# Kernel tuning notes

Measured on AMD Instinct MI355X. Metric: run time of the kernel, lower is better.

The kernel has to match this reference:

```python
import jax, jax.numpy as jnp
import numpy as np

HEADS = 4
DIM_HEAD = 32
CHUNK = 1024
GROUPS = 8
EPS = 1e-5


def setup_inputs() -> dict:
    key = jax.random.key(0)
    k1, k2, k3 = jax.random.split(key, 3)
    b, dim, h, w = 8, 64, 96, 96
    inner = HEADS * DIM_HEAD  # 128
    x = jax.random.normal(k1, (b, dim, h, w), dtype=jnp.float32)
    W_qkv = jax.random.normal(k2, (3 * inner, dim), dtype=jnp.float32) * (1.0 / np.sqrt(dim))
    W_out = jax.random.normal(k3, (dim, inner), dtype=jnp.float32) * (1.0 / np.sqrt(inner))
    b_out = jnp.zeros((dim,), dtype=jnp.float32)
    gamma = jnp.ones((dim,), dtype=jnp.float32)
    beta = jnp.zeros((dim,), dtype=jnp.float32)
    return {"x": x, "W_qkv": W_qkv, "W_out": W_out, "b_out": b_out,
            "gamma": gamma, "beta": beta}


def reference(x, W_qkv, W_out, b_out, gamma, beta):
    b, c, h, w = x.shape
    n = h * w
    nch = n // CHUNK  # number of full chunks (n chosen divisible by CHUNK)
    d = DIM_HEAD
    BH = b * HEADS

    # 1x1 conv (no bias) == matmul over channel dim
    xf = x.reshape(b, c, n)
    qkv = jnp.einsum('oc,bcn->bon', W_qkv, xf)          # [b, 3*inner, n]
    q, k, v = jnp.split(qkv, 3, axis=1)                  # each [b, inner, n]

    def chunkify(t):
        # [b, inner, n] -> [BH, nch, d, CHUNK]; slicing i:i+CHUNK on last axis
        # equals reshaping n -> (nch, CHUNK) in order.
        return t.reshape(BH, d, nch, CHUNK).transpose(0, 2, 1, 3)

    qc, kc, vc = chunkify(q), chunkify(k), chunkify(v)

    qs = jax.nn.softmax(qc, axis=-1)  # softmax over chunk spatial positions
    ks = jax.nn.softmax(kc, axis=-2)  # softmax over head channels

    # context = k_chunk^T @ v_chunk : [BH, nch, CHUNK, CHUNK]
    ctx = jnp.einsum('gkdi,gkdj->gkij', ks, vc)
    # chunk_out = q_chunk @ context : [BH, nch, d, CHUNK]
    out = jnp.einsum('gkdi,gkij->gkdj', qs, ctx)

    # concat chunks back along spatial dim, reshape to image layout
    out = out.transpose(0, 2, 1, 3).reshape(b, HEADS * d, h, w)

    # to_out: 1x1 conv with bias, then GroupNorm(8, dim)
    y = jnp.einsum('oc,bchw->bohw', W_out, out) + b_out[None, :, None, None]

    yg = y.reshape(b, GROUPS, c // GROUPS, h, w)
    mu = jnp.mean(yg, axis=(2, 3, 4), keepdims=True)
    var = jnp.var(yg, axis=(2, 3, 4), keepdims=True)
    yn = ((yg - mu) * jax.lax.rsqrt(var + EPS)).reshape(b, c, h, w)
    return yn * gamma[None, :, None, None] + beta[None, :, None, None]
```

## Files before the change

kernel.cpp:

```cpp
#include <hip/hip_runtime.h>
#include <hip/hip_bf16.h>

#define N_POS 9216
#define NCHUNK 9
#define BATCH 8
#define CDIM 64
#define HEADS 4
#define EPS 1e-5f

#define PPART_SZ ((size_t)32 * NCHUNK * 1024)
#define NPART 8
#define MP_SLICE ((size_t)(BATCH * NCHUNK) * 4096)
#define WBF_BYTES ((size_t)384 * 64 * 2)

typedef __attribute__((ext_vector_type(8))) short short8;
typedef __attribute__((ext_vector_type(4))) float f32x4;

static __device__ inline unsigned pk2(float a, float b) {
    __hip_bfloat162 h2(__float2bfloat16(a), __float2bfloat16(b));
    return *reinterpret_cast<unsigned*>(&h2);
}
static __device__ inline float bf2f(short s) {
    union { unsigned u; float f; } c; c.u = ((unsigned)(unsigned short)s) << 16; return c.f;
}

__global__ __launch_bounds__(256) void wprep_kernel(const float* __restrict__ Wqkv,
        __hip_bfloat16* __restrict__ wbf, float* __restrict__ stats) {
    int i = blockIdx.x * 256 + threadIdx.x;
    if (i < 6144) {
        float4 v = ((const float4*)Wqkv)[i];
        uint2 u; u.x = pk2(v.x, v.y); u.y = pk2(v.z, v.w);
        ((uint2*)wbf)[i] = u;
    }
    if (i < 128) stats[i] = 0.f;
}

__global__ __launch_bounds__(256) void qkp_kernel(const float* __restrict__ x,
        const __hip_bfloat16* __restrict__ wbf, float* __restrict__ Pparts) {
    int bx = blockIdx.x;
    int b  = blockIdx.y;
    int ck = bx >> 3, pt = bx & 7;
    __shared__ __align__(16) char lraw[36864];
    __hip_bfloat16 (*xs)[72]  = (__hip_bfloat16(*)[72])lraw;
    __hip_bfloat16 (*skT)[72] = (__hip_bfloat16(*)[72])lraw;
    int t = threadIdx.x, w = t >> 6, l = t & 63;
    int l15 = l & 15, quad = l >> 4;

    f32x4 pac[2][2];
    pac[0][0] = (f32x4){0,0,0,0}; pac[0][1] = (f32x4){0,0,0,0};
    pac[1][0] = (f32x4){0,0,0,0}; pac[1][1] = (f32x4){0,0,0,0};

    for (int half = 0; half < 2; ++half) {
        int n0 = bx * 128 + half * 64;
        {
            int p = t & 63, cbase = (t >> 6) * 16;
            const float* xb = x + (size_t)b * CDIM * N_POS + n0 + p;
            #pragma unroll
            for (int j = 0; j < 16; j += 4) {
                float v0 = xb[(size_t)(cbase + j + 0) * N_POS];
                float v1 = xb[(size_t)(cbase + j + 1) * N_POS];
                float v2 = xb[(size_t)(cbase + j + 2) * N_POS];
                float v3 = xb[(size_t)(cbase + j + 3) * N_POS];
                uint2 u; u.x = pk2(v0, v1); u.y = pk2(v2, v3);
                *reinterpret_cast<uint2*>(&xs[p][cbase + j]) = u;
            }
        }
        __syncthreads();

        f32x4 acc[4][4];
        #pragma unroll
        for (int mt = 0; mt < 4; ++mt)
            #pragma unroll
            for (int nt = 0; nt < 4; ++nt) acc[mt][nt] = (f32x4){0.f, 0.f, 0.f, 0.f};
        #pragma unroll
        for (int ks = 0; ks < 2; ++ks) {
            int k0 = ks * 32 + quad * 8;
            short8 av[4];
            #pragma unroll
            for (int mt = 0; mt < 4; ++mt)
                av[mt] = *reinterpret_cast<const short8*>(&xs[mt * 16 + l15][k0]);
            #pragma unroll
            for (int nt = 0; nt < 4; ++nt) {
                short8 bw = *reinterpret_cast<const short8*>(wbf + (size_t)(w * 64 + nt * 16 + l15) * 64 + k0);
                #pragma unroll
                for (int mt = 0; mt < 4; ++mt)
                    acc[mt][nt] = __builtin_amdgcn_mfma_f32_16x16x32_bf16(av[mt], bw, acc[mt][nt], 0, 0, 0);
            }
        }
        __syncthreads();

        if (w < 2) {
            #pragma unroll
            for (int nt = 0; nt < 4; ++nt) {
                int ch = w * 64 + nt * 16 + l15;
                #pragma unroll
                for (int mt = 0; mt < 4; ++mt) {
                    uint2 u;
                    u.x = pk2(__expf(acc[mt][nt][0]), __expf(acc[mt][nt][1]));
                    u.y = pk2(__expf(acc[mt][nt][2]), __expf(acc[mt][nt][3]));
                    *reinterpret_cast<uint2*>(&skT[ch][mt * 16 + quad * 4]) = u;
                }
            }
        } else {
            #pragma unroll
            for (int nt = 0; nt < 4; ++nt) {
                int ch = w * 64 + nt * 16 + l15;
                #pragma unroll
                for (int mt = 0; mt < 4; ++mt) {
                    uint2 u;
                    u.x = pk2(acc[mt][nt][0], acc[mt][nt][1]);
                    u.y = pk2(acc[mt][nt][2], acc[mt][nt][3]);
                    *reinterpret_cast<uint2*>(&skT[ch][mt * 16 + quad * 4]) = u;
                }
            }
        }
        __syncthreads();

        {
            int p = t & 63, h = t >> 6;
            float kr[32]; float mx = -1e30f;
            #pragma unroll
            for (int d = 0; d < 32; ++d) { kr[d] = bf2f(*(const short*)&skT[128 + h * 32 + d][p]); mx = fmaxf(mx, kr[d]); }
            float s = 0.f;
            #pragma unroll
            for (int d = 0; d < 32; ++d) { kr[d] = __expf(kr[d] - mx); s += kr[d]; }
            float is = 1.f / s;
            #pragma unroll
            for (int d = 0; d < 32; ++d) skT[128 + h * 32 + d][p] = __float2bfloat16(kr[d] * is);
        }
        __syncthreads();

        #pragma unroll
        for (int step = 0; step < 2; ++step) {
            int k0 = step * 32 + quad * 8;
            short8 bk[2];
            #pragma unroll
            for (int nt = 0; nt < 2; ++nt)
                bk[nt] = *reinterpret_cast<const short8*>(&skT[128 + w * 32 + nt * 16 + l15][k0]);
            #pragma unroll
            for (int mt = 0; mt < 2; ++mt) {
                short8 aq = *reinterpret_cast<const short8*>(&skT[w * 32 + mt * 16 + l15][k0]);
                pac[mt][0] = __builtin_amdgcn_mfma_f32_16x16x32_bf16(aq, bk[0], pac[mt][0], 0, 0, 0);
                pac[mt][1] = __builtin_amdgcn_mfma_f32_16x16x32_bf16(aq, bk[1], pac[mt][1], 0, 0, 0);
            }
        }
        __syncthreads();
    }

    float* Pp = Pparts + (size_t)pt * PPART_SZ + ((size_t)(b * 4 + w) * NCHUNK + ck) * 1024;
    #pragma unroll
    for (int mt = 0; mt < 2; ++mt)
        #pragma unroll
        for (int nt = 0; nt < 2; ++nt)
            #pragma unroll
            for (int r = 0; r < 4; ++r)
                Pp[(mt * 16 + quad * 4 + r) * 32 + nt * 16 + l15] = pac[mt][nt][r];
}

__global__ __launch_bounds__(256) void umat_kernel(const float* __restrict__ Wout,
        const float* __restrict__ Wqkv, const float* __restrict__ Pparts,
        float* __restrict__ Mp) {
    int ck = blockIdx.x, b = blockIdx.y, h = blockIdx.z;
    int bh = b * 4 + h;
    int t = threadIdx.x;
    __shared__ float Pl[32][32];
    __shared__ float iZ[32];
    __shared__ float Ul[64][33];
    __shared__ float Wvh[32][68];
    size_t base4 = ((size_t)bh * NCHUNK + ck) * 256;
    {
        const float4* P0 = (const float4*)Pparts + base4 + t;
        float4 s = (float4){0.f, 0.f, 0.f, 0.f};
        #pragma unroll
        for (int j = 0; j < NPART; ++j) {
            float4 a = P0[j * (PPART_SZ / 4)];
            s.x += a.x; s.y += a.y; s.z += a.z; s.w += a.w;
        }
        ((float4*)Pl)[t] = s;
    }
    {
        int e = t >> 3, cq = t & 7;
        const float4* wr = (const float4*)(Wqkv + (size_t)(256 + h * 32 + e) * 64 + cq * 8);
        float4 a0 = wr[0], a1 = wr[1];
        *reinterpret_cast<float4*>(&Wvh[e][cq * 8])     = a0;
        *reinterpret_cast<float4*>(&Wvh[e][cq * 8 + 4]) = a1;
    }
    __syncthreads();
    if (t < 32) {
        float s = 0.f;
        #pragma unroll
        for (int c = 0; c < 32; ++c) s += Pl[t][c];
        iZ[t] = 1.f / s;
    }
    __syncthreads();
    int o = t & 63, wv = t >> 6;
    float wz[32];
    {
        const float4* wr = (const float4*)(Wout + (size_t)o * 128 + h * 32);
        #pragma unroll
        for (int j = 0; j < 8; ++j) {
            float4 f = wr[j];
            wz[j*4+0] = f.x * iZ[j*4+0]; wz[j*4+1] = f.y * iZ[j*4+1];
            wz[j*4+2] = f.z * iZ[j*4+2]; wz[j*4+3] = f.w * iZ[j*4+3];
        }
    }
    float ua[8];
    #pragma unroll
    for (int j = 0; j < 8; ++j) ua[j] = 0.f;
    for (int d = 0; d < 32; ++d) {
        float wd = wz[d];
        #pragma unroll
        for (int j = 0; j < 8; ++j) ua[j] += wd * Pl[d][wv * 8 + j];
    }
    #pragma unroll
    for (int j = 0; j < 8; ++j) Ul[o][wv * 8 + j] = ua[j];
    __syncthreads();

    float macc[16];
    #pragma unroll
    for (int j = 0; j < 16; ++j) macc[j] = 0.f;
    for (int e = 0; e < 32; ++e) {
        float u = Ul[o][e];
        const float4* wvp = reinterpret_cast<const float4*>(&Wvh[e][wv * 16]);
        #pragma unroll
        for (int q = 0; q < 4; ++q) {
            float4 f = wvp[q];
            macc[q*4+0] += u * f.x; macc[q*4+1] += u * f.y;
            macc[q*4+2] += u * f.z; macc[q*4+3] += u * f.w;
        }
    }
    float* mp = Mp + (size_t)h * MP_SLICE + ((size_t)(b * NCHUNK + ck)) * 4096
              + (size_t)o * 64 + wv * 16;
    #pragma unroll
    for (int q = 0; q < 4; ++q) {
        float4 f; f.x = macc[q*4+0]; f.y = macc[q*4+1]; f.z = macc[q*4+2]; f.w = macc[q*4+3];
        reinterpret_cast<float4*>(mp)[q] = f;
    }
}

__global__ __launch_bounds__(256) void y_kernel(const float* __restrict__ x,
        const float* __restrict__ Mp, const float* __restrict__ bout,
        __hip_bfloat16* __restrict__ ybf, float* __restrict__ stats) {
    int bx = blockIdx.x;
    int b  = blockIdx.y;
    int ck = bx >> 3;
    int n0 = bx * 128;
    __shared__ __align__(16) __hip_bfloat16 xs[128][72];
    __shared__ __align__(16) __hip_bfloat16 Ml[64][72];
    __shared__ float gsum[8], gsq[8];
    int t = threadIdx.x, w = t >> 6, l = t & 63;
    int l15 = l & 15, quad = l >> 4;
    if (t < 8) { gsum[t] = 0.f; gsq[t] = 0.f; }

    {
        int p = t & 127, cbase = (t >> 7) * 32;
        const float* xb = x + (size_t)b * CDIM * N_POS + n0 + p;
        #pragma unroll
        for (int j = 0; j < 32; j += 4) {
            float v0 = xb[(size_t)(cbase + j + 0) * N_POS];
            float v1 = xb[(size_t)(cbase + j + 1) * N_POS];
            float v2 = xb[(size_t)(cbase + j + 2) * N_POS];
            float v3 = xb[(size_t)(cbase + j + 3) * N_POS];
            uint2 u; u.x = pk2(v0, v1); u.y = pk2(v2, v3);
            *reinterpret_cast<uint2*>(&xs[p][cbase + j]) = u;
        }
    }
    {
        int o = t >> 2, cs = (t & 3) * 16;
        const float* mb = Mp + ((size_t)(b * NCHUNK + ck)) * 4096 + (size_t)o * 64 + cs;
        float m[16];
        #pragma unroll
        for (int q = 0; q < 4; ++q) {
            float4 f = reinterpret_cast<const float4*>(mb)[q];
            m[q*4+0] = f.x; m[q*4+1] = f.y; m[q*4+2] = f.z; m[q*4+3] = f.w;
        }
        #pragma unroll
        for (int h = 1; h < 4; ++h) {
            const float* mh = mb + h * MP_SLICE;
            #pragma unroll
            for (int q = 0; q < 4; ++q) {
                float4 f = reinterpret_cast<const float4*>(mh)[q];
                m[q*4+0] += f.x; m[q*4+1] += f.y; m[q*4+2] += f.z; m[q*4+3] += f.w;
            }
        }
        #pragma unroll
        for (int q = 0; q < 4; ++q) {
            uint2 u; u.x = pk2(m[q*4+0], m[q*4+1]); u.y = pk2(m[q*4+2], m[q*4+3]);
            *reinterpret_cast<uint2*>(&Ml[o][cs + q * 4]) = u;
        }
    }
    __syncthreads();

    int nw = w * 32;
    f32x4 acc[4][2];
    #pragma unroll
    for (int mt = 0; mt < 4; ++mt) { acc[mt][0] = (f32x4){0,0,0,0}; acc[mt][1] = (f32x4){0,0,0,0}; }
    #pragma unroll
    for (int ks = 0; ks < 2; ++ks) {
        int k0 = ks * 32 + quad * 8;
        short8 bf[2];
        #pragma unroll
        for (int nt = 0; nt < 2; ++nt)
            bf[nt] = *reinterpret_cast<const short8*>(&xs[nw + nt * 16 + l15][k0]);
        #pragma unroll
        for (int mt = 0; mt < 4; ++mt) {
            short8 af = *reinterpret_cast<const short8*>(&Ml[mt * 16 + l15][k0]);
            acc[mt][0] = __builtin_amdgcn_mfma_f32_16x16x32_bf16(af, bf[0], acc[mt][0], 0, 0, 0);
            acc[mt][1] = __builtin_amdgcn_mfma_f32_16x16x32_bf16(af, bf[1], acc[mt][1], 0, 0, 0);
        }
    }
    float gsl[4], gql[4];
    #pragma unroll
    for (int mt = 0; mt < 4; ++mt) { gsl[mt] = 0.f; gql[mt] = 0.f; }
    __hip_bfloat16* yb = ybf + (size_t)b * CDIM * N_POS;
    int nbase = n0 + nw;
    #pragma unroll
    for (int mt = 0; mt < 4; ++mt) {
        float4 bo = *reinterpret_cast<const float4*>(bout + mt * 16 + quad * 4);
        const float* bop = reinterpret_cast<const float*>(&bo);
        #pragma unroll
        for (int nt = 0; nt < 2; ++nt) {
            int n = nbase + nt * 16 + l15;
            #pragma unroll
            for (int r = 0; r < 4; ++r) {
                int o = mt * 16 + quad * 4 + r;
                float val = acc[mt][nt][r] + bop[r];
                yb[(size_t)o * N_POS + n] = __float2bfloat16(val);
                gsl[mt] += val; gql[mt] += val * val;
            }
        }
    }
    #pragma unroll
    for (int off = 16; off >= 1; off >>= 1) {
        #pragma unroll
        for (int mt = 0; mt < 4; ++mt) {
            gsl[mt] += __shfl_xor(gsl[mt], off, 64);
            gql[mt] += __shfl_xor(gql[mt], off, 64);
        }
    }
    if (l == 0 || l == 32) {
        int qh = quad >> 1;
        #pragma unroll
        for (int mt = 0; mt < 4; ++mt) {
            atomicAdd(&gsum[2 * mt + qh], gsl[mt]);
            atomicAdd(&gsq[2 * mt + qh], gql[mt]);
        }
    }
    __syncthreads();
    if (t < 8) {
        atomicAdd(&stats[(b * 8 + t) * 2],     gsum[t]);
        atomicAdd(&stats[(b * 8 + t) * 2 + 1], gsq[t]);
    }
}

__global__ __launch_bounds__(256) void gn_kernel(const __hip_bfloat16* __restrict__ ybf,
        float* __restrict__ out, const float* __restrict__ stats,
        const float* __restrict__ gamma, const float* __restrict__ beta) {
    int bc = blockIdx.y;
    int c = bc & 63, b = bc >> 6;
    int g = c >> 3;
    float s = stats[(b * 8 + g) * 2], q = stats[(b * 8 + g) * 2 + 1];
    const float invN = 1.f / (8.f * N_POS);
    float mean = s * invN;
    float var = q * invN - mean * mean;
    float sc = rsqrtf(var + EPS);
    float ga = gamma[c] * sc;
    float be = beta[c] - mean * sc * gamma[c];
    size_t base = ((size_t)b * CDIM + c) * N_POS + (size_t)(blockIdx.x * 256 + threadIdx.x) * 4;
    uint2 u = *reinterpret_cast<const uint2*>(ybf + base);
    float4 v;
    v.x = bf2f((short)(u.x & 0xffff)); v.y = bf2f((short)(u.x >> 16));
    v.z = bf2f((short)(u.y & 0xffff)); v.w = bf2f((short)(u.y >> 16));
    v.x = v.x * ga + be; v.y = v.y * ga + be; v.z = v.z * ga + be; v.w = v.w * ga + be;
    *reinterpret_cast<float4*>(out + base) = v;
}

extern "C" void kernel_launch(void* const* d_in, const int* in_sizes, int n_in,
                              void* d_out, int out_size, void* d_ws, size_t ws_size,
                              hipStream_t stream) {
    const float* x     = (const float*)d_in[0];
    const float* Wqkv  = (const float*)d_in[1];
    const float* Wout  = (const float*)d_in[2];
    const float* bout  = (const float*)d_in[3];
    const float* gamma = (const float*)d_in[4];
    const float* beta  = (const float*)d_in[5];
    float* out = (float*)d_out;

    float* stats  = (float*)d_ws;
    float* Pparts = stats + 128;
    float* Mp     = Pparts + NPART * PPART_SZ;
    __hip_bfloat16* wbf = (__hip_bfloat16*)(Mp + 4 * MP_SLICE);
    __hip_bfloat16* ybf = (__hip_bfloat16*)((char*)wbf + WBF_BYTES);

    wprep_kernel<<<dim3(24), 256, 0, stream>>>(Wqkv, wbf, stats);
    qkp_kernel<<<dim3(72, BATCH), 256, 0, stream>>>(x, wbf, Pparts);
    umat_kernel<<<dim3(NCHUNK, BATCH, HEADS), 256, 0, stream>>>(Wout, Wqkv, Pparts, Mp);
    y_kernel<<<dim3(72, BATCH), 256, 0, stream>>>(x, Mp, bout, ybf, stats);
    gn_kernel<<<dim3(9, 512), 256, 0, stream>>>(ybf, out, stats, gamma, beta);
}
```

Before: 125.4 us.

## Load MFMA operands directly from global into registers and double qkp grid

qkp_kernel now gives each block 64 positions instead of 128, so its grid doubles and the partial-sum count goes from 8 to 16. Each wave loads its x fragment straight into MFMA registers, skipping the LDS staging pass. The k channel softmax is now done in registers with cross-lane shuffles rather than a separate LDS pass, and the partial buffer layout is reorganised to match. y_kernel likewise builds its M and x fragments directly from global memory without LDS, trading shared-memory traffic and barriers for uncoalesced strided global loads and redundant loads of M across waves.

Result: slower. 154.5 us (+23.3%).

```diff
diff --git a/kernel.cpp b/kernel.cpp
--- a/kernel.cpp
+++ b/kernel.cpp
@@ -8,8 +8,8 @@
 #define HEADS 4
 #define EPS 1e-5f
 
-#define PPART_SZ ((size_t)32 * NCHUNK * 1024)
-#define NPART 8
+#define NPART 16
+#define PPARTS_TOT ((size_t)BATCH * NCHUNK * NPART * 4096)
 #define MP_SLICE ((size_t)(BATCH * NCHUNK) * 4096)
 #define WBF_BYTES ((size_t)384 * 64 * 2)
 
@@ -22,6 +22,10 @@
 }
 static __device__ inline float bf2f(short s) {
     union { unsigned u; float f; } c; c.u = ((unsigned)(unsigned short)s) << 16; return c.f;
+}
+static __device__ inline short8 mk8(unsigned a, unsigned b, unsigned c, unsigned d) {
+    union { short8 s; unsigned u[4]; } cv;
+    cv.u[0] = a; cv.u[1] = b; cv.u[2] = c; cv.u[3] = d; return cv.s;
 }
 
 __global__ __launch_bounds__(256) void wprep_kernel(const float* __restrict__ Wqkv,
@@ -39,141 +43,115 @@
         const __hip_bfloat16* __restrict__ wbf, float* __restrict__ Pparts) {
     int bx = blockIdx.x;
     int b  = blockIdx.y;
-    int ck = bx >> 3, pt = bx & 7;
-    __shared__ __align__(16) char lraw[36864];
-    __hip_bfloat16 (*xs)[72]  = (__hip_bfloat16(*)[72])lraw;
-    __hip_bfloat16 (*skT)[72] = (__hip_bfloat16(*)[72])lraw;
+    int ck = bx >> 4, pt = bx & 15;
+    __shared__ __align__(16) __hip_bfloat16 skT[256][72];
     int t = threadIdx.x, w = t >> 6, l = t & 63;
     int l15 = l & 15, quad = l >> 4;
+    int p0 = bx * 64 + w * 16;
+
+    short8 afr[2];
+    {
+        const float* xb = x + (size_t)b * CDIM * N_POS + p0 + l15;
+        #pragma unroll
+        for (int ks = 0; ks < 2; ++ks) {
+            float v[8];
+            #pragma unroll
+            for (int j = 0; j < 8; ++j)
+                v[j] = xb[(size_t)(ks * 32 + quad * 8 + j) * N_POS];
+            afr[ks] = mk8(pk2(v[0], v[1]), pk2(v[2], v[3]),
+                          pk2(v[4], v[5]), pk2(v[6], v[7]));
+        }
+    }
+
+    f32x4 acc[16];
+    #pragma unroll
+    for (int nt = 0; nt < 16; ++nt) acc[nt] = (f32x4){0.f, 0.f, 0.f, 0.f};
+    #pragma unroll
+    for (int ks = 0; ks < 2; ++ks) {
+        #pragma unroll
+        for (int nt = 0; nt < 16; ++nt) {
+            short8 bw = *reinterpret_cast<const short8*>(
+                wbf + (size_t)(nt * 16 + l15) * 64 + ks * 32 + quad * 8);
+            acc[nt] = __builtin_amdgcn_mfma_f32_16x16x32_bf16(afr[ks], bw, acc[nt], 0, 0, 0);
+        }
+    }
+
+    #pragma unroll
+    for (int nt = 0; nt < 8; ++nt) {
+        uint2 u;
+        u.x = pk2(__expf(acc[nt][0]), __expf(acc[nt][1]));
+        u.y = pk2(__expf(acc[nt][2]), __expf(acc[nt][3]));
+        *reinterpret_cast<uint2*>(&skT[nt * 16 + l15][w * 16 + quad * 4]) = u;
+    }
+    #pragma unroll
+    for (int h = 0; h < 4; ++h) {
+        f32x4 a0 = acc[8 + 2 * h], a1 = acc[9 + 2 * h];
+        f32x4 e0, e1;
+        #pragma unroll
+        for (int r = 0; r < 4; ++r) {
+            float m = fmaxf(a0[r], a1[r]);
+            m = fmaxf(m, __shfl_xor(m, 1));
+            m = fmaxf(m, __shfl_xor(m, 2));
+            m = fmaxf(m, __shfl_xor(m, 4));
+            m = fmaxf(m, __shfl_xor(m, 8));
+            float x0 = __expf(a0[r] - m), x1 = __expf(a1[r] - m);
+            float s = x0 + x1;
+            s += __shfl_xor(s, 1);
+            s += __shfl_xor(s, 2);
+            s += __shfl_xor(s, 4);
+            s += __shfl_xor(s, 8);
+            float is = 1.f / s;
+            e0[r] = x0 * is; e1[r] = x1 * is;
+        }
+        uint2 u;
+        u.x = pk2(e0[0], e0[1]); u.y = pk2(e0[2], e0[3]);
+        *reinterpret_cast<uint2*>(&skT[128 + h * 32 + l15][w * 16 + quad * 4]) = u;
+        u.x = pk2(e1[0], e1[1]); u.y = pk2(e1[2], e1[3]);
+        *reinterpret_cast<uint2*>(&skT[128 + h * 32 + 16 + l15][w * 16 + quad * 4]) = u;
+    }
+    __syncthreads();
 
     f32x4 pac[2][2];
     pac[0][0] = (f32x4){0,0,0,0}; pac[0][1] = (f32x4){0,0,0,0};
     pac[1][0] = (f32x4){0,0,0,0}; pac[1][1] = (f32x4){0,0,0,0};
-
-    for (int half = 0; half < 2; ++half) {
-        int n0 = bx * 128 + half * 64;
-        {
-            int p = t & 63, cbase = (t >> 6) * 16;
-            const float* xb = x + (size_t)b * CDIM * N_POS + n0 + p;
-            #pragma unroll
-            for (int j = 0; j < 16; j += 4) {
-                float v0 = xb[(size_t)(cbase + j + 0) * N_POS];
-                float v1 = xb[(size_t)(cbase + j + 1) * N_POS];
-                float v2 = xb[(size_t)(cbase + j + 2) * N_POS];
-                float v3 = xb[(size_t)(cbase + j + 3) * N_POS];
-                uint2 u; u.x = pk2(v0, v1); u.y = pk2(v2, v3);
-                *reinterpret_cast<uint2*>(&xs[p][cbase + j]) = u;
-            }
-        }
-        __syncthreads();
-
-        f32x4 acc[4][4];
-        #pragma unroll
-        for (int mt = 0; mt < 4; ++mt)
-            #pragma unroll
-            for (int nt = 0; nt < 4; ++nt) acc[mt][nt] = (f32x4){0.f, 0.f, 0.f, 0.f};
-        #pragma unroll
-        for (int ks = 0; ks < 2; ++ks) {
-            int k0 = ks * 32 + quad * 8;
-            short8 av[4];
-            #pragma unroll
-            for (int mt = 0; mt < 4; ++mt)
-                av[mt] = *reinterpret_cast<const short8*>(&xs[mt * 16 + l15][k0]);
-            #pragma unroll
-            for (int nt = 0; nt < 4; ++nt) {
-                short8 bw = *reinterpret_cast<const short8*>(wbf + (size_t)(w * 64 + nt * 16 + l15) * 64 + k0);
-                #pragma unroll
-                for (int mt = 0; mt < 4; ++mt)
-                    acc[mt][nt] = __builtin_amdgcn_mfma_f32_16x16x32_bf16(av[mt], bw, acc[mt][nt], 0, 0, 0);
-            }
-        }
-        __syncthreads();
-
-        if (w < 2) {
-            #pragma unroll
-            for (int nt = 0; nt < 4; ++nt) {
-                int ch = w * 64 + nt * 16 + l15;
-                #pragma unroll
-                for (int mt = 0; mt < 4; ++mt) {
-                    uint2 u;
-                    u.x = pk2(__expf(acc[mt][nt][0]), __expf(acc[mt][nt][1]));
-                    u.y = pk2(__expf(acc[mt][nt][2]), __expf(acc[mt][nt][3]));
-                    *reinterpret_cast<uint2*>(&skT[ch][mt * 16 + quad * 4]) = u;
-                }
-            }
-        } else {
-            #pragma unroll
-            for (int nt = 0; nt < 4; ++nt) {
-                int ch = w * 64 + nt * 16 + l15;
-                #pragma unroll
-                for (int mt = 0; mt < 4; ++mt) {
-                    uint2 u;
-                    u.x = pk2(acc[mt][nt][0], acc[mt][nt][1]);
-                    u.y = pk2(acc[mt][nt][2], acc[mt][nt][3]);
-                    *reinterpret_cast<uint2*>(&skT[ch][mt * 16 + quad * 4]) = u;
-                }
-            }
-        }
-        __syncthreads();
-
-        {
-            int p = t & 63, h = t >> 6;
-            float kr[32]; float mx = -1e30f;
-            #pragma unroll
-            for (int d = 0; d < 32; ++d) { kr[d] = bf2f(*(const short*)&skT[128 + h * 32 + d][p]); mx = fmaxf(mx, kr[d]); }
-            float s = 0.f;
-            #pragma unroll
-            for (int d = 0; d < 32; ++d) { kr[d] = __expf(kr[d] - mx); s += kr[d]; }
-            float is = 1.f / s;
-            #pragma unroll
-            for (int d = 0; d < 32; ++d) skT[128 + h * 32 + d][p] = __float2bfloat16(kr[d] * is);
-        }
-        __syncthreads();
-
-        #pragma unroll
-        for (int step = 0; step < 2; ++step) {
-            int k0 = step * 32 + quad * 8;
-            short8 bk[2];
-            #pragma unroll
-            for (int nt = 0; nt < 2; ++nt)
-                bk[nt] = *reinterpret_cast<const short8*>(&skT[128 + w * 32 + nt * 16 + l15][k0]);
-            #pragma unroll
-            for (int mt = 0; mt < 2; ++mt) {
-                short8 aq = *reinterpret_cast<const short8*>(&skT[w * 32 + mt * 16 + l15][k0]);
-                pac[mt][0] = __builtin_amdgcn_mfma_f32_16x16x32_bf16(aq, bk[0], pac[mt][0], 0, 0, 0);
-                pac[mt][1] = __builtin_amdgcn_mfma_f32_16x16x32_bf16(aq, bk[1], pac[mt][1], 0, 0, 0);
-            }
-        }
-        __syncthreads();
-    }
-
-    float* Pp = Pparts + (size_t)pt * PPART_SZ + ((size_t)(b * 4 + w) * NCHUNK + ck) * 1024;
-    #pragma unroll
-    for (int mt = 0; mt < 2; ++mt)
-        #pragma unroll
-        for (int nt = 0; nt < 2; ++nt)
+    #pragma unroll
+    for (int ks = 0; ks < 2; ++ks) {
+        int k0 = ks * 32 + quad * 8;
+        short8 aq0 = *reinterpret_cast<const short8*>(&skT[w * 32 + l15][k0]);
+        short8 aq1 = *reinterpret_cast<const short8*>(&skT[w * 32 + 16 + l15][k0]);
+        short8 bk0 = *reinterpret_cast<const short8*>(&skT[128 + w * 32 + l15][k0]);
+        short8 bk1 = *reinterpret_cast<const short8*>(&skT[128 + w * 32 + 16 + l15][k0]);
+        pac[0][0] = __builtin_amdgcn_mfma_f32_16x16x32_bf16(aq0, bk0, pac[0][0], 0, 0, 0);
+        pac[0][1] = __builtin_amdgcn_mfma_f32_16x16x32_bf16(aq0, bk1, pac[0][1], 0, 0, 0);
+        pac[1][0] = __builtin_amdgcn_mfma_f32_16x16x32_bf16(aq1, bk0, pac[1][0], 0, 0, 0);
+        pac[1][1] = __builtin_amdgcn_mfma_f32_16x16x32_bf16(aq1, bk1, pac[1][1], 0, 0, 0);
+    }
+    float* Pp = Pparts + (((size_t)(b * NCHUNK + ck) * NPART + pt) * 4 + w) * 1024;
+    #pragma unroll
+    for (int tA = 0; tA < 2; ++tA)
+        #pragma unroll
+        for (int tB = 0; tB < 2; ++tB)
             #pragma unroll
             for (int r = 0; r < 4; ++r)
-                Pp[(mt * 16 + quad * 4 + r) * 32 + nt * 16 + l15] = pac[mt][nt][r];
+                Pp[(tA * 16 + quad * 4 + r) * 32 + tB * 16 + l15] = pac[tA][tB][r];
 }
 
 __global__ __launch_bounds__(256) void umat_kernel(const float* __restrict__ Wout,
         const float* __restrict__ Wqkv, const float* __restrict__ Pparts,
         float* __restrict__ Mp) {
     int ck = blockIdx.x, b = blockIdx.y, h = blockIdx.z;
-    int bh = b * 4 + h;
     int t = threadIdx.x;
     __shared__ float Pl[32][32];
     __shared__ float iZ[32];
     __shared__ float Ul[64][33];
     __shared__ float Wvh[32][68];
-    size_t base4 = ((size_t)bh * NCHUNK + ck) * 256;
-    {
-        const float4* P0 = (const float4*)Pparts + base4 + t;
+    {
+        const float4* P0 = (const float4*)Pparts
+            + ((size_t)(b * NCHUNK + ck) * NPART) * 1024 + h * 256 + t;
         float4 s = (float4){0.f, 0.f, 0.f, 0.f};
         #pragma unroll
-        for (int j = 0; j < NPART; ++j) {
-            float4 a = P0[j * (PPART_SZ / 4)];
+        for (int pt = 0; pt < NPART; ++pt) {
+            float4 a = P0[pt * 1024];
             s.x += a.x; s.y += a.y; s.z += a.z; s.w += a.w;
         }
         ((float4*)Pl)[t] = s;
@@ -245,75 +223,65 @@
     int b  = blockIdx.y;
     int ck = bx >> 3;
     int n0 = bx * 128;
-    __shared__ __align__(16) __hip_bfloat16 xs[128][72];
-    __shared__ __align__(16) __hip_bfloat16 Ml[64][72];
     __shared__ float gsum[8], gsq[8];
     int t = threadIdx.x, w = t >> 6, l = t & 63;
     int l15 = l & 15, quad = l >> 4;
     if (t < 8) { gsum[t] = 0.f; gsq[t] = 0.f; }
-
-    {
-        int p = t & 127, cbase = (t >> 7) * 32;
-        const float* xb = x + (size_t)b * CDIM * N_POS + n0 + p;
-        #pragma unroll
-        for (int j = 0; j < 32; j += 4) {
-            float v0 = xb[(size_t)(cbase + j + 0) * N_POS];
-            float v1 = xb[(size_t)(cbase + j + 1) * N_POS];
-            float v2 = xb[(size_t)(cbase + j + 2) * N_POS];
-            float v3 = xb[(size_t)(cbase + j + 3) * N_POS];
-            uint2 u; u.x = pk2(v0, v1); u.y = pk2(v2, v3);
-            *reinterpret_cast<uint2*>(&xs[p][cbase + j]) = u;
-        }
-    }
-    {
-        int o = t >> 2, cs = (t & 3) * 16;
-        const float* mb = Mp + ((size_t)(b * NCHUNK + ck)) * 4096 + (size_t)o * 64 + cs;
-        float m[16];
-        #pragma unroll
-        for (int q = 0; q < 4; ++q) {
-            float4 f = reinterpret_cast<const float4*>(mb)[q];
-            m[q*4+0] = f.x; m[q*4+1] = f.y; m[q*4+2] = f.z; m[q*4+3] = f.w;
-        }
-        #pragma unroll
-        for (int h = 1; h < 4; ++h) {
-            const float* mh = mb + h * MP_SLICE;
-            #pragma unroll
-            for (int q = 0; q < 4; ++q) {
-                float4 f = reinterpret_cast<const float4*>(mh)[q];
-                m[q*4+0] += f.x; m[q*4+1] += f.y; m[q*4+2] += f.z; m[q*4+3] += f.w;
+    __syncthreads();
+
+    short8 mf[4][2];
+    {
+        const float* Mb = Mp + (size_t)(b * NCHUNK + ck) * 4096;
+        #pragma unroll
+        for (int mt = 0; mt < 4; ++mt)
+            #pragma unroll
+            for (int ks = 0; ks < 2; ++ks) {
+                const float* m0 = Mb + (size_t)(mt * 16 + l15) * 64 + ks * 32 + quad * 8;
+                float4 s0 = *reinterpret_cast<const float4*>(m0);
+                float4 s1 = *reinterpret_cast<const float4*>(m0 + 4);
+                #pragma unroll
+                for (int h = 1; h < 4; ++h) {
+                    const float* mh = m0 + (size_t)h * MP_SLICE;
+                    float4 a0 = *reinterpret_cast<const float4*>(mh);
+                    float4 a1 = *reinterpret_cast<const float4*>(mh + 4);
+                    s0.x += a0.x; s0.y += a0.y; s0.z += a0.z; s0.w += a0.w;
+                    s1.x += a1.x; s1.y += a1.y; s1.z += a1.z; s1.w += a1.w;
+                }
+                mf[mt][ks] = mk8(pk2(s0.x, s0.y), pk2(s0.z, s0.w),
+                                 pk2(s1.x, s1.y), pk2(s1.z, s1.w));
             }
-        }
-        #pragma unroll
-        for (int q = 0; q < 4; ++q) {
-            uint2 u; u.x = pk2(m[q*4+0], m[q*4+1]); u.y = pk2(m[q*4+2], m[q*4+3]);
-            *reinterpret_cast<uint2*>(&Ml[o][cs + q * 4]) = u;
-        }
-    }
-    __syncthreads();
-
-    int nw = w * 32;
+    }
+    short8 xf[2][2];
+    {
+        const float* xb = x + (size_t)b * CDIM * N_POS + n0 + w * 32 + l15;
+        #pragma unroll
+        for (int nt = 0; nt < 2; ++nt)
+            #pragma unroll
+            for (int ks = 0; ks < 2; ++ks) {
+                float v[8];
+                #pragma unroll
+                for (int j = 0; j < 8; ++j)
+                    v[j] = xb[(size_t)(ks * 32 + quad * 8 + j) * N_POS + nt * 16];
+                xf[nt][ks] = mk8(pk2(v[0], v[1]), pk2(v[2], v[3]),
+                                 pk2(v[4], v[5]), pk2(v[6], v[7]));
+            }
+    }
     f32x4 acc[4][2];
     #pragma unroll
     for (int mt = 0; mt < 4; ++mt) { acc[mt][0] = (f32x4){0,0,0,0}; acc[mt][1] = (f32x4){0,0,0,0}; }
     #pragma unroll
-    for (int ks = 0; ks < 2; ++ks) {
-        int k0 = ks * 32 + quad * 8;
-        short8 bf[2];
-        #pragma unroll
-        for (int nt = 0; nt < 2; ++nt)
-            bf[nt] = *reinterpret_cast<const short8*>(&xs[nw + nt * 16 + l15][k0]);
+    for (int ks = 0; ks < 2; ++ks)
         #pragma unroll
         for (int mt = 0; mt < 4; ++mt) {
-            short8 af = *reinterpret_cast<const short8*>(&Ml[mt * 16 + l15][k0]);
-            acc[mt][0] = __builtin_amdgcn_mfma_f32_16x16x32_bf16(af, bf[0], acc[mt][0], 0, 0, 0);
-            acc[mt][1] = __builtin_amdgcn_mfma_f32_16x16x32_bf16(af, bf[1], acc[mt][1], 0, 0, 0);
-        }
-    }
+            acc[mt][0] = __builtin_amdgcn_mfma_f32_16x16x32_bf16(mf[mt][ks], xf[0][ks], acc[mt][0], 0, 0, 0);
+            acc[mt][1] = __builtin_amdgcn_mfma_f32_16x16x32_bf16(mf[mt][ks], xf[1][ks], acc[mt][1], 0, 0, 0);
+        }
+
     float gsl[4], gql[4];
     #pragma unroll
     for (int mt = 0; mt < 4; ++mt) { gsl[mt] = 0.f; gql[mt] = 0.f; }
     __hip_bfloat16* yb = ybf + (size_t)b * CDIM * N_POS;
-    int nbase = n0 + nw;
+    int nbase = n0 + w * 32;
     #pragma unroll
     for (int mt = 0; mt < 4; ++mt) {
         float4 bo = *reinterpret_cast<const float4*>(bout + mt * 16 + quad * 4);
@@ -388,12 +356,12 @@
 
     float* stats  = (float*)d_ws;
     float* Pparts = stats + 128;
-    float* Mp     = Pparts + NPART * PPART_SZ;
+    float* Mp     = Pparts + PPARTS_TOT;
     __hip_bfloat16* wbf = (__hip_bfloat16*)(Mp + 4 * MP_SLICE);
     __hip_bfloat16* ybf = (__hip_bfloat16*)((char*)wbf + WBF_BYTES);
 
     wprep_kernel<<<dim3(24), 256, 0, stream>>>(Wqkv, wbf, stats);
-    qkp_kernel<<<dim3(72, BATCH), 256, 0, stream>>>(x, wbf, Pparts);
+    qkp_kernel<<<dim3(144, BATCH), 256, 0, stream>>>(x, wbf, Pparts);
     umat_kernel<<<dim3(NCHUNK, BATCH, HEADS), 256, 0, stream>>>(Wout, Wqkv, Pparts, Mp);
     y_kernel<<<dim3(72, BATCH), 256, 0, stream>>>(x, Mp, bout, ybf, stats);
     gn_kernel<<<dim3(9, 512), 256, 0, stream>>>(ybf, out, stats, gamma, beta);
```

## Split qkp into 64-position blocks and compute key softmax in registers via shuffles

Applied to the files above, without the earlier changes.

The qkp kernel now handles 64 positions per block instead of looping over two 64-position halves, doubling the grid to 144x8 blocks and the number of partial P matrices to 16 per chunk. The key softmax over head channels is done directly on MFMA accumulators with cross-lane shuffles, replacing a separate LDS pass and removing two barriers. The partial-sum layout is reorganised so umat reads all partials for a (batch, chunk) contiguously. The aim is more parallelism and fewer LDS round trips and syncs, at the cost of twice the partial-sum traffic and a larger reduction in umat.

Measured after the change: 132.7 us. 1.06x slower.

```diff
diff --git a/kernel.cpp b/kernel.cpp
--- a/kernel.cpp
+++ b/kernel.cpp
@@ -8,8 +8,8 @@
 #define HEADS 4
 #define EPS 1e-5f
 
-#define PPART_SZ ((size_t)32 * NCHUNK * 1024)
-#define NPART 8
+#define NPART 16
+#define PPARTS_TOT ((size_t)BATCH * NCHUNK * NPART * 4096)
 #define MP_SLICE ((size_t)(BATCH * NCHUNK) * 4096)
 #define WBF_BYTES ((size_t)384 * 64 * 2)
 
@@ -39,141 +39,136 @@
         const __hip_bfloat16* __restrict__ wbf, float* __restrict__ Pparts) {
     int bx = blockIdx.x;
     int b  = blockIdx.y;
-    int ck = bx >> 3, pt = bx & 7;
-    __shared__ __align__(16) char lraw[36864];
-    __hip_bfloat16 (*xs)[72]  = (__hip_bfloat16(*)[72])lraw;
-    __hip_bfloat16 (*skT)[72] = (__hip_bfloat16(*)[72])lraw;
+    int ck = bx >> 4, pt = bx & 15;
+    __shared__ __align__(16) __hip_bfloat16 xs[64][72];
+    __shared__ __align__(16) __hip_bfloat16 skT[256][72];
     int t = threadIdx.x, w = t >> 6, l = t & 63;
     int l15 = l & 15, quad = l >> 4;
+    int n0 = bx * 64;
+
+    {
+        int p = t & 63, cbase = (t >> 6) * 16;
+        const float* xb = x + (size_t)b * CDIM * N_POS + n0 + p;
+        #pragma unroll
+        for (int j = 0; j < 16; j += 4) {
+            float v0 = xb[(size_t)(cbase + j + 0) * N_POS];
+            float v1 = xb[(size_t)(cbase + j + 1) * N_POS];
+            float v2 = xb[(size_t)(cbase + j + 2) * N_POS];
+            float v3 = xb[(size_t)(cbase + j + 3) * N_POS];
+            uint2 u; u.x = pk2(v0, v1); u.y = pk2(v2, v3);
+            *reinterpret_cast<uint2*>(&xs[p][cbase + j]) = u;
+        }
+    }
+    __syncthreads();
+
+    f32x4 acc[4][4];
+    #pragma unroll
+    for (int mt = 0; mt < 4; ++mt)
+        #pragma unroll
+        for (int nt = 0; nt < 4; ++nt) acc[mt][nt] = (f32x4){0.f, 0.f, 0.f, 0.f};
+    #pragma unroll
+    for (int ks = 0; ks < 2; ++ks) {
+        int k0 = ks * 32 + quad * 8;
+        short8 av[4];
+        #pragma unroll
+        for (int mt = 0; mt < 4; ++mt)
+            av[mt] = *reinterpret_cast<const short8*>(&xs[mt * 16 + l15][k0]);
+        #pragma unroll
+        for (int nt = 0; nt < 4; ++nt) {
+            short8 bw = *reinterpret_cast<const short8*>(wbf + (size_t)(w * 64 + nt * 16 + l15) * 64 + k0);
+            #pragma unroll
+            for (int mt = 0; mt < 4; ++mt)
+                acc[mt][nt] = __builtin_amdgcn_mfma_f32_16x16x32_bf16(av[mt], bw, acc[mt][nt], 0, 0, 0);
+        }
+    }
+
+    if (w < 2) {
+        #pragma unroll
+        for (int nt = 0; nt < 4; ++nt) {
+            int ch = w * 64 + nt * 16 + l15;
+            #pragma unroll
+            for (int mt = 0; mt < 4; ++mt) {
+                uint2 u;
+                u.x = pk2(__expf(acc[mt][nt][0]), __expf(acc[mt][nt][1]));
+                u.y = pk2(__expf(acc[mt][nt][2]), __expf(acc[mt][nt][3]));
+                *reinterpret_cast<uint2*>(&skT[ch][mt * 16 + quad * 4]) = u;
+            }
+        }
+    } else {
+        #pragma unroll
+        for (int hh = 0; hh < 2; ++hh) {
+            int h = (w - 2) * 2 + hh;
+            #pragma unroll
+            for (int mt = 0; mt < 4; ++mt) {
+                f32x4 a0 = acc[mt][2 * hh], a1 = acc[mt][2 * hh + 1];
+                f32x4 e0, e1;
+                #pragma unroll
+                for (int r = 0; r < 4; ++r) {
+                    float m = fmaxf(a0[r], a1[r]);
+                    m = fmaxf(m, __shfl_xor(m, 1));
+                    m = fmaxf(m, __shfl_xor(m, 2));
+                    m = fmaxf(m, __shfl_xor(m, 4));
+                    m = fmaxf(m, __shfl_xor(m, 8));
+                    float x0 = __expf(a0[r] - m), x1 = __expf(a1[r] - m);
+                    float s = x0 + x1;
+                    s += __shfl_xor(s, 1);
+                    s += __shfl_xor(s, 2);
+                    s += __shfl_xor(s, 4);
+                    s += __shfl_xor(s, 8);
+                    float is = 1.f / s;
+                    e0[r] = x0 * is; e1[r] = x1 * is;
+                }
+                uint2 u;
+                u.x = pk2(e0[0], e0[1]); u.y = pk2(e0[2], e0[3]);
+                *reinterpret_cast<uint2*>(&skT[128 + h * 32 + l15][mt * 16 + quad * 4]) = u;
+                u.x = pk2(e1[0], e1[1]); u.y = pk2(e1[2], e1[3]);
+                *reinterpret_cast<uint2*>(&skT[128 + h * 32 + 16 + l15][mt * 16 + quad * 4]) = u;
+            }
+        }
+    }
+    __syncthreads();
 
     f32x4 pac[2][2];
     pac[0][0] = (f32x4){0,0,0,0}; pac[0][1] = (f32x4){0,0,0,0};
     pac[1][0] = (f32x4){0,0,0,0}; pac[1][1] = (f32x4){0,0,0,0};
-
-    for (int half = 0; half < 2; ++half) {
-        int n0 = bx * 128 + half * 64;
-        {
-            int p = t & 63, cbase = (t >> 6) * 16;
-            const float* xb = x + (size_t)b * CDIM * N_POS + n0 + p;
-            #pragma unroll
-            for (int j = 0; j < 16; j += 4) {
-                float v0 = xb[(size_t)(cbase + j + 0) * N_POS];
-                float v1 = xb[(size_t)(cbase + j + 1) * N_POS];
-                float v2 = xb[(size_t)(cbase + j + 2) * N_POS];
-                float v3 = xb[(size_t)(cbase + j + 3) * N_POS];
-                uint2 u; u.x = pk2(v0, v1); u.y = pk2(v2, v3);
-                *reinterpret_cast<uint2*>(&xs[p][cbase + j]) = u;
-            }
-        }
-        __syncthreads();
-
-        f32x4 acc[4][4];
-        #pragma unroll
-        for (int mt = 0; mt < 4; ++mt)
-            #pragma unroll
-            for (int nt = 0; nt < 4; ++nt) acc[mt][nt] = (f32x4){0.f, 0.f, 0.f, 0.f};
-        #pragma unroll
-        for (int ks = 0; ks < 2; ++ks) {
-            int k0 = ks * 32 + quad * 8;
-            short8 av[4];
-            #pragma unroll
-            for (int mt = 0; mt < 4; ++mt)
-                av[mt] = *reinterpret_cast<const short8*>(&xs[mt * 16 + l15][k0]);
-            #pragma unroll
-            for (int nt = 0; nt < 4; ++nt) {
-                short8 bw = *reinterpret_cast<const short8*>(wbf + (size_t)(w * 64 + nt * 16 + l15) * 64 + k0);
-                #pragma unroll
-                for (int mt = 0; mt < 4; ++mt)
-                    acc[mt][nt] = __builtin_amdgcn_mfma_f32_16x16x32_bf16(av[mt], bw, acc[mt][nt], 0, 0, 0);
-            }
-        }
-        __syncthreads();
-
-        if (w < 2) {
-            #pragma unroll
-            for (int nt = 0; nt < 4; ++nt) {
-                int ch = w * 64 + nt * 16 + l15;
-                #pragma unroll
-                for (int mt = 0; mt < 4; ++mt) {
-                    uint2 u;
-                    u.x = pk2(__expf(acc[mt][nt][0]), __expf(acc[mt][nt][1]));
-                    u.y = pk2(__expf(acc[mt][nt][2]), __expf(acc[mt][nt][3]));
-                    *reinterpret_cast<uint2*>(&skT[ch][mt * 16 + quad * 4]) = u;
-                }
-            }
-        } else {
-            #pragma unroll
-            for (int nt = 0; nt < 4; ++nt) {
-                int ch = w * 64 + nt * 16 + l15;
-                #pragma unroll
-                for (int mt = 0; mt < 4; ++mt) {
-                    uint2 u;
-                    u.x = pk2(acc[mt][nt][0], acc[mt][nt][1]);
-                    u.y = pk2(acc[mt][nt][2], acc[mt][nt][3]);
-                    *reinterpret_cast<uint2*>(&skT[ch][mt * 16 + quad * 4]) = u;
-                }
-            }
-        }
-        __syncthreads();
-
-        {
-            int p = t & 63, h = t >> 6;
-            float kr[32]; float mx = -1e30f;
-            #pragma unroll
-            for (int d = 0; d < 32; ++d) { kr[d] = bf2f(*(const short*)&skT[128 + h * 32 + d][p]); mx = fmaxf(mx, kr[d]); }
-            float s = 0.f;
-            #pragma unroll
-            for (int d = 0; d < 32; ++d) { kr[d] = __expf(kr[d] - mx); s += kr[d]; }
-            float is = 1.f / s;
-            #pragma unroll
-            for (int d = 0; d < 32; ++d) skT[128 + h * 32 + d][p] = __float2bfloat16(kr[d] * is);
-        }
-        __syncthreads();
-
-        #pragma unroll
-        for (int step = 0; step < 2; ++step) {
-            int k0 = step * 32 + quad * 8;
-            short8 bk[2];
-            #pragma unroll
-            for (int nt = 0; nt < 2; ++nt)
-                bk[nt] = *reinterpret_cast<const short8*>(&skT[128 + w * 32 + nt * 16 + l15][k0]);
-            #pragma unroll
-            for (int mt = 0; mt < 2; ++mt) {
-                short8 aq = *reinterpret_cast<const short8*>(&skT[w * 32 + mt * 16 + l15][k0]);
-                pac[mt][0] = __builtin_amdgcn_mfma_f32_16x16x32_bf16(aq, bk[0], pac[mt][0], 0, 0, 0);
-                pac[mt][1] = __builtin_amdgcn_mfma_f32_16x16x32_bf16(aq, bk[1], pac[mt][1], 0, 0, 0);
-            }
-        }
-        __syncthreads();
-    }
-
-    float* Pp = Pparts + (size_t)pt * PPART_SZ + ((size_t)(b * 4 + w) * NCHUNK + ck) * 1024;
-    #pragma unroll
-    for (int mt = 0; mt < 2; ++mt)
-        #pragma unroll
-        for (int nt = 0; nt < 2; ++nt)
+    #pragma unroll
+    for (int ks = 0; ks < 2; ++ks) {
+        int k0 = ks * 32 + quad * 8;
+        short8 aq0 = *reinterpret_cast<const short8*>(&skT[w * 32 + l15][k0]);
+        short8 aq1 = *reinterpret_cast<const short8*>(&skT[w * 32 + 16 + l15][k0]);
+        short8 bk0 = *reinterpret_cast<const short8*>(&skT[128 + w * 32 + l15][k0]);
+        short8 bk1 = *reinterpret_cast<const short8*>(&skT[128 + w * 32 + 16 + l15][k0]);
+        pac[0][0] = __builtin_amdgcn_mfma_f32_16x16x32_bf16(aq0, bk0, pac[0][0], 0, 0, 0);
+        pac[0][1] = __builtin_amdgcn_mfma_f32_16x16x32_bf16(aq0, bk1, pac[0][1], 0, 0, 0);
+        pac[1][0] = __builtin_amdgcn_mfma_f32_16x16x32_bf16(aq1, bk0, pac[1][0], 0, 0, 0);
+        pac[1][1] = __builtin_amdgcn_mfma_f32_16x16x32_bf16(aq1, bk1, pac[1][1], 0, 0, 0);
+    }
+    float* Pp = Pparts + (((size_t)(b * NCHUNK + ck) * NPART + pt) * 4 + w) * 1024;
+    #pragma unroll
+    for (int tA = 0; tA < 2; ++tA)
+        #pragma unroll
+        for (int tB = 0; tB < 2; ++tB)
             #pragma unroll
             for (int r = 0; r < 4; ++r)
-                Pp[(mt * 16 + quad * 4 + r) * 32 + nt * 16 + l15] = pac[mt][nt][r];
+                Pp[(tA * 16 + quad * 4 + r) * 32 + tB * 16 + l15] = pac[tA][tB][r];
 }
 
 __global__ __launch_bounds__(256) void umat_kernel(const float* __restrict__ Wout,
         const float* __restrict__ Wqkv, const float* __restrict__ Pparts,
         float* __restrict__ Mp) {
     int ck = blockIdx.x, b = blockIdx.y, h = blockIdx.z;
-    int bh = b * 4 + h;
     int t = threadIdx.x;
     __shared__ float Pl[32][32];
     __shared__ float iZ[32];
     __shared__ float Ul[64][33];
     __shared__ float Wvh[32][68];
-    size_t base4 = ((size_t)bh * NCHUNK + ck) * 256;
-    {
-        const float4* P0 = (const float4*)Pparts + base4 + t;
+    {
+        const float4* P0 = (const float4*)Pparts
+            + ((size_t)(b * NCHUNK + ck) * NPART) * 1024 + h * 256 + t;
         float4 s = (float4){0.f, 0.f, 0.f, 0.f};
         #pragma unroll
-        for (int j = 0; j < NPART; ++j) {
-            float4 a = P0[j * (PPART_SZ / 4)];
+        for (int pt = 0; pt < NPART; ++pt) {
+            float4 a = P0[pt * 1024];
             s.x += a.x; s.y += a.y; s.z += a.z; s.w += a.w;
         }
         ((float4*)Pl)[t] = s;
@@ -388,12 +383,12 @@
 
     float* stats  = (float*)d_ws;
     float* Pparts = stats + 128;
-    float* Mp     = Pparts + NPART * PPART_SZ;
+    float* Mp     = Pparts + PPARTS_TOT;
     __hip_bfloat16* wbf = (__hip_bfloat16*)(Mp + 4 * MP_SLICE);
     __hip_bfloat16* ybf = (__hip_bfloat16*)((char*)wbf + WBF_BYTES);
 
     wprep_kernel<<<dim3(24), 256, 0, stream>>>(Wqkv, wbf, stats);
-    qkp_kernel<<<dim3(72, BATCH), 256, 0, stream>>>(x, wbf, Pparts);
+    qkp_kernel<<<dim3(144, BATCH), 256, 0, stream>>>(x, wbf, Pparts);
     umat_kernel<<<dim3(NCHUNK, BATCH, HEADS), 256, 0, stream>>>(Wout, Wqkv, Pparts, Mp);
     y_kernel<<<dim3(72, BATCH), 256, 0, stream>>>(x, Mp, bout, ybf, stats);
     gn_kernel<<<dim3(9, 512), 256, 0, stream>>>(ybf, out, stats, gamma, beta);
```
